# Performance work log

Measured on AMD Instinct MI355X. Metric: run time of the kernel, lower is better.

The kernel has to match this reference:

```python
import jax, jax.numpy as jnp
import numpy as np

DECAY = 0.99
EPS = 1e-05
DIM = 512
N_EMBED = 4096
B, H, W = 32, 32, 32


def setup_inputs() -> dict:
    key = jax.random.key(0)
    k1, k2, k3, k4, k5 = jax.random.split(key, 5)
    inp = jax.random.normal(k1, (B, H, W, DIM), dtype=jnp.float32)
    labels = jax.random.randint(k2, (B * H * W,), 0, N_EMBED)
    embed = jax.random.normal(k3, (DIM, N_EMBED), dtype=jnp.float32)
    cluster_size = jax.random.uniform(k4, (N_EMBED,), dtype=jnp.float32)
    embed_avg = jax.random.normal(k5, (DIM, N_EMBED), dtype=jnp.float32)
    return {"input": inp, "labels": labels, "embed": embed,
            "cluster_size": cluster_size, "embed_avg": embed_avg}


def reference(input, labels, embed, cluster_size, embed_avg):
    dim, n_embed = embed.shape
    flatten = input.reshape(-1, dim)                      # [N, dim]

    # codebook gather (F.embedding on embed.T)
    embed_ind = labels.reshape(input.shape[:-1])          # [B, H, W]
    quantize = jnp.take(embed.T, embed_ind, axis=0)       # [B, H, W, dim]

    # training EMA update: onehot-scatter expressed as segment_sum
    # (math identical to flatten.T @ one_hot(labels))
    onehot_sum = jnp.zeros((n_embed,), flatten.dtype).at[labels].add(1.0)   # [n_embed]
    embed_sum = jax.ops.segment_sum(flatten, labels, num_segments=n_embed).T  # [dim, n_embed]

    new_cluster_size = cluster_size * DECAY + (1.0 - DECAY) * onehot_sum
    new_embed_avg = embed_avg * DECAY + (1.0 - DECAY) * embed_sum
    n = new_cluster_size.sum()
    cs = (new_cluster_size + EPS) / (n + n_embed * EPS) * n
    new_embed = new_embed_avg / cs[None, :]

    diff = jnp.mean((jax.lax.stop_gradient(quantize) - input) ** 2)
    return (quantize, diff, embed_ind, new_embed, new_cluster_size, new_embed_avg)
```

## Files before the change

kernel.cpp:

```cpp
#include <hip/hip_runtime.h>

#define DIMV   512
#define NEMB   4096
#define NTOK   32768
#define TOTAL  (NTOK * DIMV)

#define OFF_Q    0u
#define OFF_DIFF 16777216u
#define OFF_IND  16777217u
#define OFF_NE   16809985u
#define OFF_NCS  18907137u
#define OFF_NEA  18911233u

#define WS_SUMT    0u
#define WS_BINCNT  2097152u
#define WS_BINST   2101248u
#define WS_SORTED  2105344u
#define WS_DIFF    2138112u
#define WS_NSUM    2138113u

#define DECAYF 0.99f
#define OMDF   0.01f
#define EPSF   1e-5f

__global__ __launch_bounds__(1024) void k_sort(
        const int*   __restrict__ labels,
        const float* __restrict__ cluster_size,
        float* __restrict__ out,
        int*   __restrict__ bin_count,
        int*   __restrict__ bin_start,
        int*   __restrict__ sorted_tok,
        float* __restrict__ n_sum,
        float* __restrict__ diff_acc) {
    __shared__ int   hist[NEMB];
    __shared__ int   part[1024];
    __shared__ float fred[1024];
    int t = threadIdx.x;
    #pragma unroll
    for (int i = 0; i < 4; ++i) hist[t + i * 1024] = 0;
    __syncthreads();

    int4 labs[8];
    #pragma unroll
    for (int i = 0; i < 8; ++i) {
        int n4 = (i * 1024 + t) * 4;
        int4 l = *(const int4*)(labels + n4);
        labs[i] = l;
        out[OFF_IND + n4 + 0] = (float)l.x;
        out[OFF_IND + n4 + 1] = (float)l.y;
        out[OFF_IND + n4 + 2] = (float)l.z;
        out[OFF_IND + n4 + 3] = (float)l.w;
        atomicAdd(&hist[l.x], 1); atomicAdd(&hist[l.y], 1);
        atomicAdd(&hist[l.z], 1); atomicAdd(&hist[l.w], 1);
    }
    __syncthreads();

    int c[4]; int csum = 0; float nl = 0.f;
    #pragma unroll
    for (int i = 0; i < 4; ++i) {
        int b = t * 4 + i;
        int cc = hist[b];
        c[i] = csum; csum += cc;
        bin_count[b] = cc;
        float ncs = cluster_size[b] * DECAYF + OMDF * (float)cc;
        out[OFF_NCS + b] = ncs;
        nl += ncs;
    }
    part[t] = csum;
    fred[t] = nl;
    __syncthreads();
    for (int o = 1; o < 1024; o <<= 1) {
        int v = (t >= o) ? part[t - o] : 0;
        __syncthreads();
        part[t] += v;
        __syncthreads();
    }
    for (int o = 512; o > 0; o >>= 1) {
        if (t < o) fred[t] += fred[t + o];
        __syncthreads();
    }
    if (t == 0) { n_sum[0] = fred[0]; diff_acc[0] = 0.f; }

    int base = part[t] - csum;
    int bs[4];
    #pragma unroll
    for (int i = 0; i < 4; ++i) {
        bs[i] = base + c[i];
        bin_start[t * 4 + i] = bs[i];
    }
    __syncthreads();
    #pragma unroll
    for (int i = 0; i < 4; ++i) hist[t * 4 + i] = bs[i];
    __syncthreads();

    #pragma unroll
    for (int i = 0; i < 8; ++i) {
        int n4 = (i * 1024 + t) * 4;
        int4 l = labs[i];
        sorted_tok[atomicAdd(&hist[l.x], 1)] = n4 + 0;
        sorted_tok[atomicAdd(&hist[l.y], 1)] = n4 + 1;
        sorted_tok[atomicAdd(&hist[l.z], 1)] = n4 + 2;
        sorted_tok[atomicAdd(&hist[l.w], 1)] = n4 + 3;
    }
}

#define CHUNK 128
__global__ __launch_bounds__(256) void k_perlabel(
        const float* __restrict__ inp,
        const float* __restrict__ embed,
        const int*   __restrict__ sorted_tok,
        const int*   __restrict__ bin_start,
        const int*   __restrict__ bin_count,
        float* __restrict__ out,
        float* __restrict__ sumT,
        float* __restrict__ diff_acc) {
    int e    = blockIdx.x;
    int t    = threadIdx.x;
    int wave = t >> 6;
    int lane = t & 63;
    int d0   = lane << 3;

    float qa0 = embed[(size_t)(d0 + 0) * NEMB + e];
    float qa1 = embed[(size_t)(d0 + 1) * NEMB + e];
    float qa2 = embed[(size_t)(d0 + 2) * NEMB + e];
    float qa3 = embed[(size_t)(d0 + 3) * NEMB + e];
    float qb0 = embed[(size_t)(d0 + 4) * NEMB + e];
    float qb1 = embed[(size_t)(d0 + 5) * NEMB + e];
    float qb2 = embed[(size_t)(d0 + 6) * NEMB + e];
    float qb3 = embed[(size_t)(d0 + 7) * NEMB + e];
    float4 qa = make_float4(qa0, qa1, qa2, qa3);
    float4 qb = make_float4(qb0, qb1, qb2, qb3);

    int start = bin_start[e];
    int cnt   = bin_count[e];

    __shared__ int toks[CHUNK];
    float4 sa = make_float4(0, 0, 0, 0);
    float4 sb = make_float4(0, 0, 0, 0);
    float dacc = 0.f;

    for (int base = 0; base < cnt; base += CHUNK) {
        int m = min(CHUNK, cnt - base);
        if (t < m) toks[t] = sorted_tok[start + base + t];
        __syncthreads();
        #pragma unroll 2
        for (int i = wave; i < m; i += 4) {
            int n = toks[i];
            const float* row = inp + (size_t)n * DIMV + d0;
            float4 xa = *(const float4*)(row);
            float4 xb = *(const float4*)(row + 4);
            sa.x += xa.x; sa.y += xa.y; sa.z += xa.z; sa.w += xa.w;
            sb.x += xb.x; sb.y += xb.y; sb.z += xb.z; sb.w += xb.w;
            float t0 = qa.x - xa.x, t1 = qa.y - xa.y, t2 = qa.z - xa.z, t3 = qa.w - xa.w;
            float u0 = qb.x - xb.x, u1 = qb.y - xb.y, u2 = qb.z - xb.z, u3 = qb.w - xb.w;
            dacc += t0 * t0 + t1 * t1 + t2 * t2 + t3 * t3
                  + u0 * u0 + u1 * u1 + u2 * u2 + u3 * u3;
            float* orow = out + OFF_Q + (size_t)n * DIMV + d0;
            *(float4*)(orow)     = qa;
            *(float4*)(orow + 4) = qb;
        }
        __syncthreads();
    }

    __shared__ float ssum[4][DIMV];
    *(float4*)(&ssum[wave][d0])     = sa;
    *(float4*)(&ssum[wave][d0 + 4]) = sb;
    __syncthreads();
    for (int d = t; d < DIMV; d += 256) {
        sumT[(size_t)e * DIMV + d] =
            ssum[0][d] + ssum[1][d] + ssum[2][d] + ssum[3][d];
    }
    __shared__ float sh[256];
    sh[t] = dacc;
    __syncthreads();
    for (int o = 128; o > 0; o >>= 1) {
        if (t < o) sh[t] += sh[t + o];
        __syncthreads();
    }
    if (t == 0) atomicAdd(diff_acc, sh[0]);
}

__global__ __launch_bounds__(256) void k_trans_final(
        const float* __restrict__ embed_avg,
        const float* __restrict__ sumT,
        const float* __restrict__ n_sum,
        const float* __restrict__ diff_acc,
        float* __restrict__ out) {
    __shared__ float tile[32][33];
    int tx = threadIdx.x & 31;
    int ty = threadIdx.x >> 5;
    int e0 = (blockIdx.x & 127) << 5;
    int d0 = (blockIdx.x >> 7) << 5;
    for (int i = 0; i < 4; ++i) {
        int er = ty + i * 8;
        tile[er][tx] = sumT[(size_t)(e0 + er) * DIMV + d0 + tx];
    }
    __syncthreads();
    float nsum = n_sum[0];
    float ncs  = out[OFF_NCS + e0 + tx];
    float cs   = (ncs + EPSF) / (nsum + (float)NEMB * EPSF) * nsum;
    float inv  = 1.0f / cs;
    for (int i = 0; i < 4; ++i) {
        int dr = d0 + ty + i * 8;
        size_t o = (size_t)dr * NEMB + e0 + tx;
        float val = DECAYF * embed_avg[o] + OMDF * tile[tx][ty + i * 8];
        out[OFF_NEA + o] = val;
        out[OFF_NE + o]  = val * inv;
    }
    if (blockIdx.x == 0 && threadIdx.x == 0)
        out[OFF_DIFF] = diff_acc[0] * (1.0f / (float)TOTAL);
}

extern "C" void kernel_launch(void* const* d_in, const int* in_sizes, int n_in,
                              void* d_out, int out_size, void* d_ws, size_t ws_size,
                              hipStream_t stream) {
    const float* inp          = (const float*)d_in[0];
    const int*   labels       = (const int*)  d_in[1];
    const float* embed        = (const float*)d_in[2];
    const float* cluster_size = (const float*)d_in[3];
    const float* embed_avg    = (const float*)d_in[4];
    float* out = (float*)d_out;

    float* wsf        = (float*)d_ws;
    float* sumT       = wsf + WS_SUMT;
    int*   bin_count  = (int*)(wsf + WS_BINCNT);
    int*   bin_start  = (int*)(wsf + WS_BINST);
    int*   sorted_tok = (int*)(wsf + WS_SORTED);
    float* diff_acc   = wsf + WS_DIFF;
    float* n_sum      = wsf + WS_NSUM;

    k_sort      <<<1,    1024, 0, stream>>>(labels, cluster_size, out,
                                            bin_count, bin_start, sorted_tok,
                                            n_sum, diff_acc);
    k_perlabel  <<<4096, 256,  0, stream>>>(inp, embed, sorted_tok, bin_start,
                                            bin_count, out, sumT, diff_acc);
    k_trans_final<<<2048,256,  0, stream>>>(embed_avg, sumT, n_sum, diff_acc, out);
}
```

Measured before the change: 231.7 us.

## Assign one wave per codebook entry with shuffled indices and prefetched rows

The per-label kernel now gives each 64-lane wave its own embedding entry instead of splitting one entry across four waves of a block. Token indices are loaded into registers and broadcast with shuffles rather than staged in shared memory. The next row is prefetched while the current one is accumulated. All block-level syncs and the shared-memory reductions are removed, and the diff partial is reduced with wave shuffles. The cost is that each entry is handled by a single wave, so per-wave memory parallelism drops and the 8 codebook loads stay strided.

After: 232.5 us. About the same (+0.3%).

```diff
diff --git a/kernel.cpp b/kernel.cpp
--- a/kernel.cpp
+++ b/kernel.cpp
@@ -82,15 +82,12 @@
     if (t == 0) { n_sum[0] = fred[0]; diff_acc[0] = 0.f; }
 
     int base = part[t] - csum;
-    int bs[4];
-    #pragma unroll
-    for (int i = 0; i < 4; ++i) {
-        bs[i] = base + c[i];
-        bin_start[t * 4 + i] = bs[i];
-    }
-    __syncthreads();
-    #pragma unroll
-    for (int i = 0; i < 4; ++i) hist[t * 4 + i] = bs[i];
+    #pragma unroll
+    for (int i = 0; i < 4; ++i)
+        bin_start[t * 4 + i] = base + c[i];
+    __syncthreads();
+    #pragma unroll
+    for (int i = 0; i < 4; ++i) hist[t * 4 + i] = base + c[i];
     __syncthreads();
 
     #pragma unroll
@@ -104,7 +101,6 @@
     }
 }
 
-#define CHUNK 128
 __global__ __launch_bounds__(256) void k_perlabel(
         const float* __restrict__ inp,
         const float* __restrict__ embed,
@@ -114,70 +110,65 @@
         float* __restrict__ out,
         float* __restrict__ sumT,
         float* __restrict__ diff_acc) {
-    int e    = blockIdx.x;
     int t    = threadIdx.x;
     int wave = t >> 6;
     int lane = t & 63;
+    int e    = (blockIdx.x << 2) | wave;
     int d0   = lane << 3;
 
-    float qa0 = embed[(size_t)(d0 + 0) * NEMB + e];
-    float qa1 = embed[(size_t)(d0 + 1) * NEMB + e];
-    float qa2 = embed[(size_t)(d0 + 2) * NEMB + e];
-    float qa3 = embed[(size_t)(d0 + 3) * NEMB + e];
-    float qb0 = embed[(size_t)(d0 + 4) * NEMB + e];
-    float qb1 = embed[(size_t)(d0 + 5) * NEMB + e];
-    float qb2 = embed[(size_t)(d0 + 6) * NEMB + e];
-    float qb3 = embed[(size_t)(d0 + 7) * NEMB + e];
-    float4 qa = make_float4(qa0, qa1, qa2, qa3);
-    float4 qb = make_float4(qb0, qb1, qb2, qb3);
+    const float* col = embed + e;
+    float4 qa, qb;
+    qa.x = col[(size_t)(d0 + 0) * NEMB];
+    qa.y = col[(size_t)(d0 + 1) * NEMB];
+    qa.z = col[(size_t)(d0 + 2) * NEMB];
+    qa.w = col[(size_t)(d0 + 3) * NEMB];
+    qb.x = col[(size_t)(d0 + 4) * NEMB];
+    qb.y = col[(size_t)(d0 + 5) * NEMB];
+    qb.z = col[(size_t)(d0 + 6) * NEMB];
+    qb.w = col[(size_t)(d0 + 7) * NEMB];
 
     int start = bin_start[e];
     int cnt   = bin_count[e];
 
-    __shared__ int toks[CHUNK];
     float4 sa = make_float4(0, 0, 0, 0);
     float4 sb = make_float4(0, 0, 0, 0);
     float dacc = 0.f;
 
-    for (int base = 0; base < cnt; base += CHUNK) {
-        int m = min(CHUNK, cnt - base);
-        if (t < m) toks[t] = sorted_tok[start + base + t];
-        __syncthreads();
-        #pragma unroll 2
-        for (int i = wave; i < m; i += 4) {
-            int n = toks[i];
-            const float* row = inp + (size_t)n * DIMV + d0;
-            float4 xa = *(const float4*)(row);
-            float4 xb = *(const float4*)(row + 4);
+    for (int base = 0; base < cnt; base += 64) {
+        int m = min(64, cnt - base);
+        int idx = (lane < m) ? sorted_tok[start + base + lane] : 0;
+        int ncur = __shfl(idx, 0);
+        const float* r = inp + (size_t)ncur * DIMV + d0;
+        float4 xa = *(const float4*)(r);
+        float4 xb = *(const float4*)(r + 4);
+        for (int i = 1; i <= m; ++i) {
+            float4 pa, pb;
+            int nprev = ncur;
+            if (i < m) {
+                ncur = __shfl(idx, i);
+                const float* r2 = inp + (size_t)ncur * DIMV + d0;
+                pa = *(const float4*)(r2);
+                pb = *(const float4*)(r2 + 4);
+            }
             sa.x += xa.x; sa.y += xa.y; sa.z += xa.z; sa.w += xa.w;
             sb.x += xb.x; sb.y += xb.y; sb.z += xb.z; sb.w += xb.w;
             float t0 = qa.x - xa.x, t1 = qa.y - xa.y, t2 = qa.z - xa.z, t3 = qa.w - xa.w;
             float u0 = qb.x - xb.x, u1 = qb.y - xb.y, u2 = qb.z - xb.z, u3 = qb.w - xb.w;
             dacc += t0 * t0 + t1 * t1 + t2 * t2 + t3 * t3
                   + u0 * u0 + u1 * u1 + u2 * u2 + u3 * u3;
-            float* orow = out + OFF_Q + (size_t)n * DIMV + d0;
+            float* orow = out + OFF_Q + (size_t)nprev * DIMV + d0;
             *(float4*)(orow)     = qa;
             *(float4*)(orow + 4) = qb;
+            if (i < m) { xa = pa; xb = pb; }
         }
-        __syncthreads();
-    }
-
-    __shared__ float ssum[4][DIMV];
-    *(float4*)(&ssum[wave][d0])     = sa;
-    *(float4*)(&ssum[wave][d0 + 4]) = sb;
-    __syncthreads();
-    for (int d = t; d < DIMV; d += 256) {
-        sumT[(size_t)e * DIMV + d] =
-            ssum[0][d] + ssum[1][d] + ssum[2][d] + ssum[3][d];
-    }
-    __shared__ float sh[256];
-    sh[t] = dacc;
-    __syncthreads();
-    for (int o = 128; o > 0; o >>= 1) {
-        if (t < o) sh[t] += sh[t + o];
-        __syncthreads();
-    }
-    if (t == 0) atomicAdd(diff_acc, sh[0]);
+    }
+
+    float* so = sumT + (size_t)e * DIMV + d0;
+    *(float4*)(so)     = sa;
+    *(float4*)(so + 4) = sb;
+
+    for (int o = 32; o > 0; o >>= 1) dacc += __shfl_down(dacc, o);
+    if (lane == 0) atomicAdd(diff_acc, dacc);
 }
 
 __global__ __launch_bounds__(256) void k_trans_final(
@@ -232,7 +223,7 @@
     k_sort      <<<1,    1024, 0, stream>>>(labels, cluster_size, out,
                                             bin_count, bin_start, sorted_tok,
                                             n_sum, diff_acc);
-    k_perlabel  <<<4096, 256,  0, stream>>>(inp, embed, sorted_tok, bin_start,
+    k_perlabel  <<<1024, 256,  0, stream>>>(inp, embed, sorted_tok, bin_start,
                                             bin_count, out, sumT, diff_acc);
     k_trans_final<<<2048,256,  0, stream>>>(embed_avg, sumT, n_sum, diff_acc, out);
 }
```
